# Optimization experiments

Hardware: AMD Instinct MI355X
Metric: run time of the kernel (lower is better)

Reference implementation:

```python
import jax, jax.numpy as jnp
import numpy as np

B, S, E, H = 2, 2048, 1024, 16
DH = E // H  # 64


def setup_inputs() -> dict:
    key = jax.random.key(0)
    ks = jax.random.split(key, 10)
    scale = 1.0 / np.sqrt(E)
    x = jax.random.normal(ks[0], (B, S, E), dtype=jnp.float32)
    mask = jax.random.randint(ks[1], (B, S), 0, 2, dtype=jnp.int32)
    # per-head Q/K/V projections stacked: [H, E, DH] (x @ W, torch Linear transposed)
    wq = jax.random.normal(ks[2], (H, E, DH), dtype=jnp.float32) * scale
    wk = jax.random.normal(ks[3], (H, E, DH), dtype=jnp.float32) * scale
    wv = jax.random.normal(ks[4], (H, E, DH), dtype=jnp.float32) * scale
    bq = jax.random.normal(ks[5], (H, DH), dtype=jnp.float32) * scale
    bk = jax.random.normal(ks[6], (H, DH), dtype=jnp.float32) * scale
    bv = jax.random.normal(ks[7], (H, DH), dtype=jnp.float32) * scale
    wo = jax.random.normal(ks[8], (E, E), dtype=jnp.float32) * scale
    bo = jax.random.normal(ks[9], (E,), dtype=jnp.float32) * scale
    return {"x": x, "mask": mask, "wq": wq, "bq": bq, "wk": wk, "bk": bk,
            "wv": wv, "bv": bv, "wo": wo, "bo": bo}


def reference(x, mask, wq, bq, wk, bk, wv, bv, wo, bo):
    # q,k,v: [B, H, S, DH]
    q = jnp.einsum('bse,hed->bhsd', x, wq) + bq[None, :, None, :]
    k = jnp.einsum('bse,hed->bhsd', x, wk) + bk[None, :, None, :]
    v = jnp.einsum('bse,hed->bhsd', x, wv) + bv[None, :, None, :]
    scores = jnp.einsum('bhsd,bhtd->bhst', q, k) / np.sqrt(DH)
    # padding mask on key axis: mask==0 -> -1e9 (as in masked_fill)
    scores = jnp.where(mask[:, None, None, :] == 0, jnp.float32(-1e9), scores)
    attn = jax.nn.softmax(scores, axis=-1)
    o = jnp.einsum('bhst,bhtd->bhsd', attn, v)
    # concat heads -> [B, S, E], then output projection
    o = o.transpose(0, 2, 1, 3).reshape(B, S, E)
    return o @ wo + bo
```

## Files before the change

### kernel.cpp

```cpp
#include <hip/hip_runtime.h>
#include <hip/hip_bf16.h>
#include <math.h>

#define Bsz 2
#define Ssz 2048
#define Esz 1024
#define Hsz 16
#define DHsz 64

typedef __bf16 bf16_t;
typedef __attribute__((ext_vector_type(8))) __bf16 bf16x8;
typedef __attribute__((ext_vector_type(4))) float f32x4;

typedef unsigned int u32;
typedef const __attribute__((address_space(1))) u32* gptr_t;
typedef __attribute__((address_space(3))) u32* lptr_t;

#if __has_builtin(__builtin_amdgcn_exp2f)
#define EXP2F(x) __builtin_amdgcn_exp2f(x)
#else
#define EXP2F(x) __expf((x)*0.69314718f)
#endif

__device__ __forceinline__ bf16_t to_bf16(float f) {
  union { float f; unsigned u; } v; v.f = f;
  unsigned r = (v.u + 0x7FFF + ((v.u >> 16) & 1)) >> 16;
  union { unsigned short s; bf16_t b; } o; o.s = (unsigned short)r;
  return o.b;
}

__device__ __forceinline__ unsigned pack2_rtz(float a, float b) {
#if __has_builtin(__builtin_amdgcn_perm)
  return __builtin_amdgcn_perm(__float_as_uint(b), __float_as_uint(a), 0x07060302u);
#else
  return (__float_as_uint(a) >> 16) | (__float_as_uint(b) & 0xFFFF0000u);
#endif
}

__device__ __forceinline__ unsigned pack2(float a, float b) {
  union { float f; unsigned u; } x, y; x.f = a; y.f = b;
  unsigned ra = (x.u + 0x7FFF + ((x.u >> 16) & 1)) >> 16;
  unsigned rb = (y.u + 0x7FFF + ((y.u >> 16) & 1)) >> 16;
  return ra | (rb << 16);
}

__device__ __forceinline__ f32x4 mfma16(bf16x8 a, bf16x8 b, f32x4 c) {
  return __builtin_amdgcn_mfma_f32_16x16x32_bf16(a, b, c, 0, 0, 0);
}

__device__ __forceinline__ void gload16(void* lds, const void* g) {
  __builtin_amdgcn_global_load_lds((gptr_t)g, (lptr_t)lds, 16, 0, 0);
}

#define PREP_CAST 4096
#define PREP_MASK 4112
__global__ __launch_bounds__(256) void prep(
    const float* __restrict__ x, const int* __restrict__ mask,
    const float* __restrict__ wq, const float* __restrict__ wk,
    const float* __restrict__ wv, const float* __restrict__ wo,
    bf16_t* __restrict__ xb, bf16_t* __restrict__ mb,
    bf16_t* __restrict__ wAll, bf16_t* __restrict__ wAllV, bf16_t* __restrict__ woT) {
  __shared__ bf16_t lT[64 * 72];
  const int bid = blockIdx.x, t = threadIdx.x;
  if (bid < PREP_CAST) {
    const int i = bid * 256 + t;
    float4 v = ((const float4*)x)[i];
    uint2 o; o.x = pack2(v.x, v.y); o.y = pack2(v.z, v.w);
    ((uint2*)xb)[i] = o;
  } else if (bid < PREP_MASK) {
    const int i = (bid - PREP_CAST) * 256 + t;
    mb[i] = to_bf16(mask[i] ? 1.0f : 0.0f);
  } else {
    const int t2 = bid - PREP_MASK;
    const int et = t2 & 15, h = (t2 >> 4) & 15, z = t2 >> 8;
    const float* src; int srcLD; bf16_t* dst;
    if (z == 0)      { src = wq + ((size_t)h * Esz + et * 64) * DHsz; srcLD = DHsz; dst = wAll  + (size_t)(h * 64) * Esz; }
    else if (z == 1) { src = wk + ((size_t)h * Esz + et * 64) * DHsz; srcLD = DHsz; dst = wAll  + (size_t)(1024 + h * 64) * Esz; }
    else if (z == 2) { src = wv + ((size_t)h * Esz + et * 64) * DHsz; srcLD = DHsz; dst = wAllV + (size_t)(h * 64) * Esz; }
    else             { src = wo + (size_t)(et * 64) * Esz + h * 64;   srcLD = Esz;  dst = woT   + (size_t)(h * 64) * Esz; }
#pragma unroll
    for (int rr = 0; rr < 4; rr++) {
      int er = rr * 16 + (t >> 4);
      int dc = (t & 15) * 4;
      float4 v = *(const float4*)&src[(size_t)er * srcLD + dc];
      lT[(dc + 0) * 72 + er] = to_bf16(v.x);
      lT[(dc + 1) * 72 + er] = to_bf16(v.y);
      lT[(dc + 2) * 72 + er] = to_bf16(v.z);
      lT[(dc + 3) * 72 + er] = to_bf16(v.w);
    }
    __syncthreads();
#pragma unroll
    for (int rr = 0; rr < 2; rr++) {
      int d = rr * 32 + (t >> 3);
      int e8 = (t & 7) * 8;
      bf16x8 o = *(const bf16x8*)&lT[d * 72 + e8];
      *(bf16x8*)&dst[(size_t)d * Esz + et * 64 + e8] = o;
    }
  }
}

template <int TM, int TN>
__device__ __forceinline__ void gemm_core(
    const bf16_t* __restrict__ Ab, const bf16_t* __restrict__ Bb, int K,
    bf16_t* lA, bf16_t* lB, f32x4 (&acc)[TM / 32][TN / 32]) {
  const int tid = threadIdx.x, lane = tid & 63, wvi = tid >> 6;
  const int g = lane >> 4, c = lane & 15, cw = c & 7;
  const int lrow = lane >> 3, sg = lane & 7;
  const int wm = wvi >> 1, wn = wvi & 1;
  for (int kc = 0; kc < K; kc += 64) {
#pragma unroll
    for (int j = 0; j < TM / 32; j++) {
      const int base = (j * 4 + wvi) * 8;
      const int row = base + lrow;
      gload16(lA + base * 64, Ab + (size_t)row * K + kc + ((sg ^ (row & 7)) * 8));
    }
#pragma unroll
    for (int j = 0; j < TN / 32; j++) {
      const int base = (j * 4 + wvi) * 8;
      const int row = base + lrow;
      gload16(lB + base * 64, Bb + (size_t)row * K + kc + ((sg ^ (row & 7)) * 8));
    }
    __syncthreads();
#pragma unroll
    for (int ksp = 0; ksp < 2; ksp++) {
      const int kg = (ksp * 4 + g) ^ cw;
      bf16x8 af[TM / 32], bfr[TN / 32];
#pragma unroll
      for (int mt = 0; mt < TM / 32; mt++)
        af[mt] = *(const bf16x8*)&lA[(wm * (TM / 2) + mt * 16 + c) * 64 + kg * 8];
#pragma unroll
      for (int nt = 0; nt < TN / 32; nt++)
        bfr[nt] = *(const bf16x8*)&lB[(wn * (TN / 2) + nt * 16 + c) * 64 + kg * 8];
#pragma unroll
      for (int mt = 0; mt < TM / 32; mt++)
#pragma unroll
        for (int nt = 0; nt < TN / 32; nt++)
          acc[mt][nt] = mfma16(af[mt], bfr[nt], acc[mt][nt]);
    }
    __syncthreads();
  }
}

__global__ __launch_bounds__(256, 3) void qkv_gemm(
    const bf16_t* __restrict__ xb, const bf16_t* __restrict__ wAll,
    const bf16_t* __restrict__ wAllV, const bf16_t* __restrict__ mb,
    const float* __restrict__ bq, const float* __restrict__ bk,
    const float* __restrict__ bv,
    bf16_t* __restrict__ qb, bf16_t* __restrict__ kb, bf16_t* __restrict__ vTb) {
  __shared__ alignas(16) bf16_t lA[128 * 64];
  __shared__ alignas(16) bf16_t lB[128 * 64];
  const int bid = blockIdx.x;
  const int lane = threadIdx.x & 63, wvi = threadIdx.x >> 6;
  const int g = lane >> 4, c = lane & 15;
  const int wm = wvi >> 1, wn = wvi & 1;
  f32x4 acc[4][4] = {};
  if (bid < 512) {
    const int Mb = (bid & 31) * 128, Nb = (bid >> 5) * 128;
    gemm_core<128, 128>(xb + (size_t)Mb * Esz, wAll + (size_t)Nb * Esz, Esz, lA, lB, acc);
#pragma unroll
    for (int nt = 0; nt < 4; nt++) {
      const int col = Nb + wn * 64 + nt * 16 + c;
      const int which = col >> 10, h = (col >> 6) & 15, d = col & 63;
      const float bias = (which ? bk : bq)[h * DHsz + d];
      const float scale = which ? 1.0f : 0.18033688011112042f;
      bf16_t* dst = which ? kb : qb;
#pragma unroll
      for (int mt = 0; mt < 4; mt++)
#pragma unroll
        for (int r = 0; r < 4; r++) {
          const int row = Mb + wm * 64 + mt * 16 + g * 4 + r;
          const int b = row >> 11, s = row & 2047;
          dst[(((size_t)(b * Hsz + h)) * Ssz + s) * DHsz + d] =
              to_bf16((acc[mt][nt][r] + bias) * scale);
        }
    }
  } else {
    const int t2 = bid - 512;
    const int Mb = (t2 & 7) * 128, Nb = ((t2 >> 3) & 15) * 128, b = t2 >> 7;
    gemm_core<128, 128>(wAllV + (size_t)Mb * Esz, xb + ((size_t)(b * Ssz) + Nb) * Esz,
                        Esz, lA, lB, acc);
#pragma unroll
    for (int nt = 0; nt < 4; nt++) {
      const int s = Nb + wn * 64 + nt * 16 + c;
      const float mval = (float)mb[b * Ssz + s];
#pragma unroll
      for (int mt = 0; mt < 4; mt++)
#pragma unroll
        for (int r = 0; r < 4; r++) {
          const int m = Mb + wm * 64 + mt * 16 + g * 4 + r;
          vTb[((size_t)(b * 1024 + m)) * Ssz + s] = to_bf16((acc[mt][nt][r] + bv[m]) * mval);
        }
    }
  }
}

__global__ __launch_bounds__(128, 2) void flash_attn(
    const bf16_t* __restrict__ qb, const bf16_t* __restrict__ kb,
    const bf16_t* __restrict__ vTb, const bf16_t* __restrict__ mb,
    bf16_t* __restrict__ Ob) {
  __shared__ alignas(16) bf16_t lK[2][64 * 64];
  __shared__ alignas(16) bf16_t lP[2][32 * 64];

  const int h = blockIdx.x, qt = blockIdx.y, b = blockIdx.z;
  const size_t bh = (size_t)(b * Hsz + h);
  const int tid = threadIdx.x, lane = tid & 63, wv = tid >> 6;
  const int g = lane >> 4, c = lane & 15, cw = c & 7;
  const int lrow = lane >> 3, sg = lane & 7;

  const bf16_t* Kbase = kb + bh * (size_t)Ssz * DHsz;
  const bf16_t* Vlane = vTb + bh * (size_t)DHsz * Ssz + c * Ssz + g * 8;
  const bf16_t* mbb = mb + b * Ssz + g * 8;

  bf16x8 qf[2][2];
  const bf16_t* Qbase = qb + (bh * Ssz + qt * 64 + wv * 32) * DHsz;
#pragma unroll
  for (int qsub = 0; qsub < 2; qsub++)
#pragma unroll
    for (int ksp = 0; ksp < 2; ksp++)
      qf[qsub][ksp] = *(const bf16x8*)&Qbase[(qsub * 16 + c) * DHsz + ksp * 32 + g * 8];

  f32x4 o[2][4] = {};
  f32x4 lac[2] = {};

  auto stage = [&](int tc, int buf) {
#pragma unroll
    for (int j = 0; j < 4; j++) {
      const int rowbase = wv * 32 + j * 8;
      const int row = rowbase + lrow;
      const int lg = sg ^ (row & 7);
      gload16(&lK[buf][rowbase * 64], Kbase + ((size_t)(tc * 64 + row)) * DHsz + lg * 8);
    }
  };

  auto loadVM = [&](int tc, bf16x8 (&vf)[2][4], bf16x8 (&mfr)[2]) {
    const bf16_t* vp = Vlane + tc * 64;
#pragma unroll
    for (int ksp = 0; ksp < 2; ksp++) {
      mfr[ksp] = *(const bf16x8*)&mbb[tc * 64 + ksp * 32];
#pragma unroll
      for (int dt = 0; dt < 4; dt++)
        vf[ksp][dt] = *(const bf16x8*)&vp[dt * 16 * Ssz + ksp * 32];
    }
  };

  auto compute = [&](int buf, bf16x8 (&vf)[2][4], bf16x8 (&mfr)[2]) {
    const bf16_t* Kt = lK[buf];
    f32x4 st[2][4] = {};
#pragma unroll
    for (int ksp = 0; ksp < 2; ksp++) {
      const int kgr = (ksp * 4 + g) ^ cw;
#pragma unroll
      for (int nt = 0; nt < 4; nt++) {
        bf16x8 kf = *(const bf16x8*)&Kt[(nt * 16 + c) * 64 + kgr * 8];
        st[0][nt] = mfma16(kf, qf[0][ksp], st[0][nt]);
        st[1][nt] = mfma16(kf, qf[1][ksp], st[1][nt]);
      }
    }
#pragma unroll
    for (int qsub = 0; qsub < 2; qsub++)
#pragma unroll
      for (int nt = 0; nt < 4; nt++) {
        float p0 = EXP2F(st[qsub][nt][0]);
        float p1 = EXP2F(st[qsub][nt][1]);
        float p2 = EXP2F(st[qsub][nt][2]);
        float p3 = EXP2F(st[qsub][nt][3]);
        const int pg = (nt * 2 + (g >> 1)) ^ cw;
        uint2 pv; pv.x = pack2_rtz(p0, p1); pv.y = pack2_rtz(p2, p3);
        *(uint2*)&lP[wv][(qsub * 16 + c) * 64 + pg * 8 + (g & 1) * 4] = pv;
      }
#pragma unroll
    for (int ksp = 0; ksp < 2; ksp++) {
      const int kgr = (ksp * 4 + g) ^ cw;
      bf16x8 pf0 = *(const bf16x8*)&lP[wv][(0 * 16 + c) * 64 + kgr * 8];
      bf16x8 pf1 = *(const bf16x8*)&lP[wv][(1 * 16 + c) * 64 + kgr * 8];
      lac[0] = mfma16(pf0, mfr[ksp], lac[0]);
      lac[1] = mfma16(pf1, mfr[ksp], lac[1]);
#pragma unroll
      for (int dt = 0; dt < 4; dt++) {
        o[0][dt] = mfma16(pf0, vf[ksp][dt], o[0][dt]);
        o[1][dt] = mfma16(pf1, vf[ksp][dt], o[1][dt]);
      }
    }
  };

  bf16x8 vA[2][4], vB[2][4], mA[2], mB[2];
  stage(0, 0);
  loadVM(0, vA, mA);
  __syncthreads();
  for (int tc = 0; tc < 32; tc += 2) {
    stage(tc + 1, 1);
    loadVM(tc + 1, vB, mB);
    compute(0, vA, mA);
    __syncthreads();
    if (tc + 2 < 32) {
      stage(tc + 2, 0);
      loadVM(tc + 2, vA, mA);
    }
    compute(1, vB, mB);
    __syncthreads();
  }

#pragma unroll
  for (int qsub = 0; qsub < 2; qsub++)
#pragma unroll
    for (int r = 0; r < 4; r++) {
      const int row = qsub * 16 + g * 4 + r;
      const float linv = 1.0f / fmaxf(lac[qsub][r], 1e-30f);
      const size_t orow = (size_t)(b * Ssz + qt * 64 + wv * 32 + row) * Esz + h * DHsz;
#pragma unroll
      for (int dt = 0; dt < 4; dt++)
        Ob[orow + dt * 16 + c] = to_bf16(o[qsub][dt][r] * linv);
    }
}

__global__ __launch_bounds__(256, 3) void out_gemm(
    const bf16_t* __restrict__ Ob, const bf16_t* __restrict__ woT,
    const float* __restrict__ bo, float* __restrict__ out) {
  __shared__ alignas(16) bf16_t lA[128 * 64];
  __shared__ alignas(16) bf16_t lB[64 * 64];
  f32x4 acc[4][2] = {};
  const int Mb = blockIdx.x * 128, Nb = blockIdx.y * 64;
  gemm_core<128, 64>(Ob + (size_t)Mb * Esz, woT + (size_t)Nb * Esz, Esz, lA, lB, acc);
  const int lane = threadIdx.x & 63, wvi = threadIdx.x >> 6;
  const int g = lane >> 4, c = lane & 15;
  const int wm = wvi >> 1, wn = wvi & 1;
#pragma unroll
  for (int nt = 0; nt < 2; nt++) {
    const int col = Nb + wn * 32 + nt * 16 + c;
    const float bias = bo[col];
#pragma unroll
    for (int mt = 0; mt < 4; mt++)
#pragma unroll
      for (int r = 0; r < 4; r++) {
        const int row = Mb + wm * 64 + mt * 16 + g * 4 + r;
        out[(size_t)row * Esz + col] = acc[mt][nt][r] + bias;
      }
  }
}

extern "C" void kernel_launch(void* const* d_in, const int* in_sizes, int n_in,
                              void* d_out, int out_size, void* d_ws, size_t ws_size,
                              hipStream_t stream) {
  const float* x = (const float*)d_in[0];
  const int* mask = (const int*)d_in[1];
  const float* wq = (const float*)d_in[2];
  const float* bq = (const float*)d_in[3];
  const float* wk = (const float*)d_in[4];
  const float* bk = (const float*)d_in[5];
  const float* wv = (const float*)d_in[6];
  const float* bv = (const float*)d_in[7];
  const float* wo = (const float*)d_in[8];
  const float* bo = (const float*)d_in[9];
  float* out = (float*)d_out;

  char* ws = (char*)d_ws;
  size_t off = 0;
  auto take = [&](size_t bytes) -> char* {
    char* p = ws + off;
    off += (bytes + 255) & ~(size_t)255;
    return p;
  };
  bf16_t* xb    = (bf16_t*)take((size_t)Bsz * Ssz * Esz * 2);
  bf16_t* wAll  = (bf16_t*)take((size_t)2 * Esz * Esz * 2);
  bf16_t* wAllV = (bf16_t*)take((size_t)Esz * Esz * 2);
  bf16_t* woT   = (bf16_t*)take((size_t)Esz * Esz * 2);
  bf16_t* qb    = (bf16_t*)take((size_t)Bsz * Hsz * Ssz * DHsz * 2);
  bf16_t* kb    = (bf16_t*)take((size_t)Bsz * Hsz * Ssz * DHsz * 2);
  bf16_t* vTb   = (bf16_t*)take((size_t)Bsz * Hsz * Ssz * DHsz * 2);
  bf16_t* Ob    = (bf16_t*)take((size_t)Bsz * Ssz * Esz * 2);
  bf16_t* mb    = (bf16_t*)take((size_t)Bsz * Ssz * 2);

  prep<<<5136, 256, 0, stream>>>(x, mask, wq, wk, wv, wo, xb, mb, wAll, wAllV, woT);
  qkv_gemm<<<768, 256, 0, stream>>>(xb, wAll, wAllV, mb, bq, bk, bv, qb, kb, vTb);
  flash_attn<<<dim3(Hsz, Ssz / 64, Bsz), 128, 0, stream>>>(qb, kb, vTb, mb, Ob);
  out_gemm<<<dim3(Bsz * Ssz / 128, Esz / 64), 256, 0, stream>>>(Ob, woT, bo, out);
}
```

Before: 211.8 us.

## Split attention key range across wave pairs and reduce partials through LDS

The flash attention kernel now uses 256 threads per block. Two wave pairs each process half of the key sequence (1024 keys) for the same 64 query rows, and their unnormalized output and row-sum accumulators are merged through shared memory at the end. K tiles are read directly from global memory into registers instead of being staged through double-buffered LDS with syncs. This is meant to raise parallelism and occupancy and remove per-tile barriers, at the cost of an extra reduction step, uncoalesced-style direct K loads, and no explicit prefetch pipelining.

New measurement: 264.6 us. +24.9%, slower.

```diff
diff --git a/kernel.cpp b/kernel.cpp
--- a/kernel.cpp
+++ b/kernel.cpp
@@ -194,25 +194,28 @@
   }
 }
 
-__global__ __launch_bounds__(128, 2) void flash_attn(
+__global__ __launch_bounds__(256, 4) void flash_attn(
     const bf16_t* __restrict__ qb, const bf16_t* __restrict__ kb,
     const bf16_t* __restrict__ vTb, const bf16_t* __restrict__ mb,
     bf16_t* __restrict__ Ob) {
-  __shared__ alignas(16) bf16_t lK[2][64 * 64];
-  __shared__ alignas(16) bf16_t lP[2][32 * 64];
+  __shared__ alignas(16) char smem[2 * 64 * 40 * 4];
+  bf16_t* lP = (bf16_t*)smem;
+  float* cbuf = (float*)smem;
 
   const int h = blockIdx.x, qt = blockIdx.y, b = blockIdx.z;
   const size_t bh = (size_t)(b * Hsz + h);
   const int tid = threadIdx.x, lane = tid & 63, wv = tid >> 6;
+  const int qh = wv & 1;
+  const int p = wv >> 1;
   const int g = lane >> 4, c = lane & 15, cw = c & 7;
-  const int lrow = lane >> 3, sg = lane & 7;
-
-  const bf16_t* Kbase = kb + bh * (size_t)Ssz * DHsz;
-  const bf16_t* Vlane = vTb + bh * (size_t)DHsz * Ssz + c * Ssz + g * 8;
-  const bf16_t* mbb = mb + b * Ssz + g * 8;
+
+  const bf16_t* Kbase = kb + (bh * Ssz + (size_t)p * 1024) * DHsz;
+  const bf16_t* Vlane = vTb + bh * (size_t)DHsz * Ssz + (size_t)c * Ssz + p * 1024 + g * 8;
+  const bf16_t* mbb = mb + b * Ssz + p * 1024 + g * 8;
+  bf16_t* lPw = lP + wv * (32 * 64);
 
   bf16x8 qf[2][2];
-  const bf16_t* Qbase = qb + (bh * Ssz + qt * 64 + wv * 32) * DHsz;
+  const bf16_t* Qbase = qb + (bh * Ssz + qt * 64 + qh * 32) * DHsz;
 #pragma unroll
   for (int qsub = 0; qsub < 2; qsub++)
 #pragma unroll
@@ -222,40 +225,30 @@
   f32x4 o[2][4] = {};
   f32x4 lac[2] = {};
 
-  auto stage = [&](int tc, int buf) {
-#pragma unroll
-    for (int j = 0; j < 4; j++) {
-      const int rowbase = wv * 32 + j * 8;
-      const int row = rowbase + lrow;
-      const int lg = sg ^ (row & 7);
-      gload16(&lK[buf][rowbase * 64], Kbase + ((size_t)(tc * 64 + row)) * DHsz + lg * 8);
-    }
-  };
-
-  auto loadVM = [&](int tc, bf16x8 (&vf)[2][4], bf16x8 (&mfr)[2]) {
+  for (int tc = 0; tc < 16; ++tc) {
+    const bf16_t* Kt = Kbase + (size_t)(tc * 64) * DHsz;
+    f32x4 st[2][4] = {};
+#pragma unroll
+    for (int ksp = 0; ksp < 2; ksp++) {
+      bf16x8 kf[4];
+#pragma unroll
+      for (int nt = 0; nt < 4; nt++)
+        kf[nt] = *(const bf16x8*)&Kt[(size_t)(nt * 16 + c) * DHsz + ksp * 32 + g * 8];
+#pragma unroll
+      for (int nt = 0; nt < 4; nt++) {
+        st[0][nt] = mfma16(kf[nt], qf[0][ksp], st[0][nt]);
+        st[1][nt] = mfma16(kf[nt], qf[1][ksp], st[1][nt]);
+      }
+    }
+
     const bf16_t* vp = Vlane + tc * 64;
-#pragma unroll
-    for (int ksp = 0; ksp < 2; ksp++) {
-      mfr[ksp] = *(const bf16x8*)&mbb[tc * 64 + ksp * 32];
-#pragma unroll
-      for (int dt = 0; dt < 4; dt++)
-        vf[ksp][dt] = *(const bf16x8*)&vp[dt * 16 * Ssz + ksp * 32];
-    }
-  };
-
-  auto compute = [&](int buf, bf16x8 (&vf)[2][4], bf16x8 (&mfr)[2]) {
-    const bf16_t* Kt = lK[buf];
-    f32x4 st[2][4] = {};
-#pragma unroll
-    for (int ksp = 0; ksp < 2; ksp++) {
-      const int kgr = (ksp * 4 + g) ^ cw;
-#pragma unroll
-      for (int nt = 0; nt < 4; nt++) {
-        bf16x8 kf = *(const bf16x8*)&Kt[(nt * 16 + c) * 64 + kgr * 8];
-        st[0][nt] = mfma16(kf, qf[0][ksp], st[0][nt]);
-        st[1][nt] = mfma16(kf, qf[1][ksp], st[1][nt]);
-      }
-    }
+    bf16x8 vfA[4], vfB[4], mf[2];
+    mf[0] = *(const bf16x8*)&mbb[tc * 64];
+    mf[1] = *(const bf16x8*)&mbb[tc * 64 + 32];
+#pragma unroll
+    for (int dt = 0; dt < 4; dt++)
+      vfA[dt] = *(const bf16x8*)&vp[dt * 16 * Ssz];
+
 #pragma unroll
     for (int qsub = 0; qsub < 2; qsub++)
 #pragma unroll
@@ -266,51 +259,73 @@
         float p3 = EXP2F(st[qsub][nt][3]);
         const int pg = (nt * 2 + (g >> 1)) ^ cw;
         uint2 pv; pv.x = pack2_rtz(p0, p1); pv.y = pack2_rtz(p2, p3);
-        *(uint2*)&lP[wv][(qsub * 16 + c) * 64 + pg * 8 + (g & 1) * 4] = pv;
-      }
-#pragma unroll
-    for (int ksp = 0; ksp < 2; ksp++) {
-      const int kgr = (ksp * 4 + g) ^ cw;
-      bf16x8 pf0 = *(const bf16x8*)&lP[wv][(0 * 16 + c) * 64 + kgr * 8];
-      bf16x8 pf1 = *(const bf16x8*)&lP[wv][(1 * 16 + c) * 64 + kgr * 8];
-      lac[0] = mfma16(pf0, mfr[ksp], lac[0]);
-      lac[1] = mfma16(pf1, mfr[ksp], lac[1]);
+        *(uint2*)&lPw[(qsub * 16 + c) * 64 + pg * 8 + (g & 1) * 4] = pv;
+      }
+
+#pragma unroll
+    for (int dt = 0; dt < 4; dt++)
+      vfB[dt] = *(const bf16x8*)&vp[dt * 16 * Ssz + 32];
+
+    {
+      const int kgr0 = g ^ cw;
+      bf16x8 pf0 = *(const bf16x8*)&lPw[(0 * 16 + c) * 64 + kgr0 * 8];
+      bf16x8 pf1 = *(const bf16x8*)&lPw[(1 * 16 + c) * 64 + kgr0 * 8];
+      lac[0] = mfma16(pf0, mf[0], lac[0]);
+      lac[1] = mfma16(pf1, mf[0], lac[1]);
 #pragma unroll
       for (int dt = 0; dt < 4; dt++) {
-        o[0][dt] = mfma16(pf0, vf[ksp][dt], o[0][dt]);
-        o[1][dt] = mfma16(pf1, vf[ksp][dt], o[1][dt]);
-      }
-    }
-  };
-
-  bf16x8 vA[2][4], vB[2][4], mA[2], mB[2];
-  stage(0, 0);
-  loadVM(0, vA, mA);
+        o[0][dt] = mfma16(pf0, vfA[dt], o[0][dt]);
+        o[1][dt] = mfma16(pf1, vfA[dt], o[1][dt]);
+      }
+    }
+    {
+      const int kgr1 = (4 + g) ^ cw;
+      bf16x8 pf0 = *(const bf16x8*)&lPw[(0 * 16 + c) * 64 + kgr1 * 8];
+      bf16x8 pf1 = *(const bf16x8*)&lPw[(1 * 16 + c) * 64 + kgr1 * 8];
+      lac[0] = mfma16(pf0, mf[1], lac[0]);
+      lac[1] = mfma16(pf1, mf[1], lac[1]);
+#pragma unroll
+      for (int dt = 0; dt < 4; dt++) {
+        o[0][dt] = mfma16(pf0, vfB[dt], o[0][dt]);
+        o[1][dt] = mfma16(pf1, vfB[dt], o[1][dt]);
+      }
+    }
+  }
+
   __syncthreads();
-  for (int tc = 0; tc < 32; tc += 2) {
-    stage(tc + 1, 1);
-    loadVM(tc + 1, vB, mB);
-    compute(0, vA, mA);
-    __syncthreads();
-    if (tc + 2 < 32) {
-      stage(tc + 2, 0);
-      loadVM(tc + 2, vA, mA);
-    }
-    compute(1, vB, mB);
-    __syncthreads();
-  }
-
-#pragma unroll
-  for (int qsub = 0; qsub < 2; qsub++)
-#pragma unroll
-    for (int r = 0; r < 4; r++) {
-      const int row = qsub * 16 + g * 4 + r;
-      const float linv = 1.0f / fmaxf(lac[qsub][r], 1e-30f);
-      const size_t orow = (size_t)(b * Ssz + qt * 64 + wv * 32 + row) * Esz + h * DHsz;
+  if (p == 1) {
+    float* cb = cbuf + ((size_t)(qh * 64 + lane)) * 40;
+#pragma unroll
+    for (int qsub = 0; qsub < 2; qsub++)
 #pragma unroll
       for (int dt = 0; dt < 4; dt++)
-        Ob[orow + dt * 16 + c] = to_bf16(o[qsub][dt][r] * linv);
-    }
+        *(f32x4*)&cb[(qsub * 4 + dt) * 4] = o[qsub][dt];
+    *(f32x4*)&cb[32] = lac[0];
+    *(f32x4*)&cb[36] = lac[1];
+  }
+  __syncthreads();
+  if (p == 0) {
+    const float* cb = cbuf + ((size_t)(qh * 64 + lane)) * 40;
+#pragma unroll
+    for (int qsub = 0; qsub < 2; qsub++)
+#pragma unroll
+      for (int dt = 0; dt < 4; dt++)
+        o[qsub][dt] += *(const f32x4*)&cb[(qsub * 4 + dt) * 4];
+    lac[0] += *(const f32x4*)&cb[32];
+    lac[1] += *(const f32x4*)&cb[36];
+
+#pragma unroll
+    for (int qsub = 0; qsub < 2; qsub++)
+#pragma unroll
+      for (int r = 0; r < 4; r++) {
+        const int row = qsub * 16 + g * 4 + r;
+        const float linv = 1.0f / fmaxf(lac[qsub][r], 1e-30f);
+        const size_t orow = (size_t)(b * Ssz + qt * 64 + qh * 32 + row) * Esz + h * DHsz;
+#pragma unroll
+        for (int dt = 0; dt < 4; dt++)
+          Ob[orow + dt * 16 + c] = to_bf16(o[qsub][dt][r] * linv);
+      }
+  }
 }
 
 __global__ __launch_bounds__(256, 3) void out_gemm(
@@ -372,6 +387,6 @@
 
   prep<<<5136, 256, 0, stream>>>(x, mask, wq, wk, wv, wo, xb, mb, wAll, wAllV, woT);
   qkv_gemm<<<768, 256, 0, stream>>>(xb, wAll, wAllV, mb, bq, bk, bv, qb, kb, vTb);
-  flash_attn<<<dim3(Hsz, Ssz / 64, Bsz), 128, 0, stream>>>(qb, kb, vTb, mb, Ob);
+  flash_attn<<<dim3(Hsz, Ssz / 64, Bsz), 256, 0, stream>>>(qb, kb, vTb, mb, Ob);
   out_gemm<<<dim3(Bsz * Ssz / 128, Esz / 64), 256, 0, stream>>>(Ob, woT, bo, out);
 }
```

## Split attention key range across two wave pairs and reduce partials in LDS

Applied to the files above, without the earlier changes.

The flash attention block grows from 2 to 4 waves. Each pair of waves handles half of the key sequence (1024 keys) for the same 64 queries, so each wave runs half as many loop iterations. The second pair writes its unnormalised output and row-sum partials to shared memory, and the first pair adds them before normalising and storing. This doubles the waves in flight per block to hide latency, at the cost of a larger shared-memory footprint, an extra reduction step, and possibly lower block occupancy per CU.

After: 226.6 us. +7.0%, slower.

```diff
diff --git a/kernel.cpp b/kernel.cpp
--- a/kernel.cpp
+++ b/kernel.cpp
@@ -194,25 +194,31 @@
   }
 }
 
-__global__ __launch_bounds__(128, 2) void flash_attn(
+__global__ __launch_bounds__(256, 2) void flash_attn(
     const bf16_t* __restrict__ qb, const bf16_t* __restrict__ kb,
     const bf16_t* __restrict__ vTb, const bf16_t* __restrict__ mb,
     bf16_t* __restrict__ Ob) {
-  __shared__ alignas(16) bf16_t lK[2][64 * 64];
-  __shared__ alignas(16) bf16_t lP[2][32 * 64];
+  __shared__ alignas(16) char smem[49152];
+  bf16_t* lK = (bf16_t*)smem;
+  bf16_t* lP = (bf16_t*)(smem + 32768);
+  float* cbuf = (float*)smem;
 
   const int h = blockIdx.x, qt = blockIdx.y, b = blockIdx.z;
   const size_t bh = (size_t)(b * Hsz + h);
   const int tid = threadIdx.x, lane = tid & 63, wv = tid >> 6;
+  const int qh = wv & 1;
+  const int p = wv >> 1;
   const int g = lane >> 4, c = lane & 15, cw = c & 7;
   const int lrow = lane >> 3, sg = lane & 7;
 
-  const bf16_t* Kbase = kb + bh * (size_t)Ssz * DHsz;
-  const bf16_t* Vlane = vTb + bh * (size_t)DHsz * Ssz + c * Ssz + g * 8;
-  const bf16_t* mbb = mb + b * Ssz + g * 8;
+  const bf16_t* Kbase = kb + (bh * Ssz + (size_t)p * 1024) * DHsz;
+  const bf16_t* Vlane = vTb + bh * (size_t)DHsz * Ssz + (size_t)c * Ssz + p * 1024 + g * 8;
+  const bf16_t* mbb = mb + b * Ssz + p * 1024 + g * 8;
+  bf16_t* lKp = lK + p * 2 * 4096;
+  bf16_t* lPw = lP + wv * (32 * 64);
 
   bf16x8 qf[2][2];
-  const bf16_t* Qbase = qb + (bh * Ssz + qt * 64 + wv * 32) * DHsz;
+  const bf16_t* Qbase = qb + (bh * Ssz + qt * 64 + qh * 32) * DHsz;
 #pragma unroll
   for (int qsub = 0; qsub < 2; qsub++)
 #pragma unroll
@@ -225,10 +231,10 @@
   auto stage = [&](int tc, int buf) {
 #pragma unroll
     for (int j = 0; j < 4; j++) {
-      const int rowbase = wv * 32 + j * 8;
+      const int rowbase = qh * 32 + j * 8;
       const int row = rowbase + lrow;
-      const int lg = sg ^ (row & 7);
-      gload16(&lK[buf][rowbase * 64], Kbase + ((size_t)(tc * 64 + row)) * DHsz + lg * 8);
+      gload16(&lKp[buf * 4096 + rowbase * 64],
+              Kbase + ((size_t)(tc * 64 + row)) * DHsz + (sg ^ lrow) * 8);
     }
   };
 
@@ -244,7 +250,7 @@
   };
 
   auto compute = [&](int buf, bf16x8 (&vf)[2][4], bf16x8 (&mfr)[2]) {
-    const bf16_t* Kt = lK[buf];
+    const bf16_t* Kt = lKp + buf * 4096;
     f32x4 st[2][4] = {};
 #pragma unroll
     for (int ksp = 0; ksp < 2; ksp++) {
@@ -266,13 +272,13 @@
         float p3 = EXP2F(st[qsub][nt][3]);
         const int pg = (nt * 2 + (g >> 1)) ^ cw;
         uint2 pv; pv.x = pack2_rtz(p0, p1); pv.y = pack2_rtz(p2, p3);
-        *(uint2*)&lP[wv][(qsub * 16 + c) * 64 + pg * 8 + (g & 1) * 4] = pv;
+        *(uint2*)&lPw[(qsub * 16 + c) * 64 + pg * 8 + (g & 1) * 4] = pv;
       }
 #pragma unroll
     for (int ksp = 0; ksp < 2; ksp++) {
       const int kgr = (ksp * 4 + g) ^ cw;
-      bf16x8 pf0 = *(const bf16x8*)&lP[wv][(0 * 16 + c) * 64 + kgr * 8];
-      bf16x8 pf1 = *(const bf16x8*)&lP[wv][(1 * 16 + c) * 64 + kgr * 8];
+      bf16x8 pf0 = *(const bf16x8*)&lPw[(0 * 16 + c) * 64 + kgr * 8];
+      bf16x8 pf1 = *(const bf16x8*)&lPw[(1 * 16 + c) * 64 + kgr * 8];
       lac[0] = mfma16(pf0, mfr[ksp], lac[0]);
       lac[1] = mfma16(pf1, mfr[ksp], lac[1]);
 #pragma unroll
@@ -287,12 +293,12 @@
   stage(0, 0);
   loadVM(0, vA, mA);
   __syncthreads();
-  for (int tc = 0; tc < 32; tc += 2) {
+  for (int tc = 0; tc < 16; tc += 2) {
     stage(tc + 1, 1);
     loadVM(tc + 1, vB, mB);
     compute(0, vA, mA);
     __syncthreads();
-    if (tc + 2 < 32) {
+    if (tc + 2 < 16) {
       stage(tc + 2, 0);
       loadVM(tc + 2, vA, mA);
     }
@@ -300,17 +306,39 @@
     __syncthreads();
   }
 
-#pragma unroll
-  for (int qsub = 0; qsub < 2; qsub++)
-#pragma unroll
-    for (int r = 0; r < 4; r++) {
-      const int row = qsub * 16 + g * 4 + r;
-      const float linv = 1.0f / fmaxf(lac[qsub][r], 1e-30f);
-      const size_t orow = (size_t)(b * Ssz + qt * 64 + wv * 32 + row) * Esz + h * DHsz;
+  if (p == 1) {
+    float* cb = cbuf + ((size_t)(qh * 64 + lane)) * 40;
+#pragma unroll
+    for (int qsub = 0; qsub < 2; qsub++)
 #pragma unroll
       for (int dt = 0; dt < 4; dt++)
-        Ob[orow + dt * 16 + c] = to_bf16(o[qsub][dt][r] * linv);
-    }
+        *(f32x4*)&cb[(qsub * 4 + dt) * 4] = o[qsub][dt];
+    *(f32x4*)&cb[32] = lac[0];
+    *(f32x4*)&cb[36] = lac[1];
+  }
+  __syncthreads();
+  if (p == 0) {
+    const float* cb = cbuf + ((size_t)(qh * 64 + lane)) * 40;
+#pragma unroll
+    for (int qsub = 0; qsub < 2; qsub++)
+#pragma unroll
+      for (int dt = 0; dt < 4; dt++)
+        o[qsub][dt] += *(const f32x4*)&cb[(qsub * 4 + dt) * 4];
+    lac[0] += *(const f32x4*)&cb[32];
+    lac[1] += *(const f32x4*)&cb[36];
+
+#pragma unroll
+    for (int qsub = 0; qsub < 2; qsub++)
+#pragma unroll
+      for (int r = 0; r < 4; r++) {
+        const int row = qsub * 16 + g * 4 + r;
+        const float linv = 1.0f / fmaxf(lac[qsub][r], 1e-30f);
+        const size_t orow = (size_t)(b * Ssz + qt * 64 + qh * 32 + row) * Esz + h * DHsz;
+#pragma unroll
+        for (int dt = 0; dt < 4; dt++)
+          Ob[orow + dt * 16 + c] = to_bf16(o[qsub][dt][r] * linv);
+      }
+  }
 }
 
 __global__ __launch_bounds__(256, 3) void out_gemm(
@@ -372,6 +400,6 @@
 
   prep<<<5136, 256, 0, stream>>>(x, mask, wq, wk, wv, wo, xb, mb, wAll, wAllV, woT);
   qkv_gemm<<<768, 256, 0, stream>>>(xb, wAll, wAllV, mb, bq, bk, bv, qb, kb, vTb);
-  flash_attn<<<dim3(Hsz, Ssz / 64, Bsz), 128, 0, stream>>>(qb, kb, vTb, mb, Ob);
+  flash_attn<<<dim3(Hsz, Ssz / 64, Bsz), 256, 0, stream>>>(qb, kb, vTb, mb, Ob);
   out_gemm<<<dim3(Bsz * Ssz / 128, Esz / 64), 256, 0, stream>>>(Ob, woT, bo, out);
 }
```
